# Kernel tuning notes

Hardware: AMD Instinct MI355X
Metric: run time of the kernel (lower is better)

## Reference

```python
import jax, jax.numpy as jnp
import numpy as np

EUCLIDEAN_DIM = 6
B = 1024


def _build_tables(n):
    # CGA: basis vectors e1..en, e+, e-, diagonal metric (+1)*(n+1), (-1)
    d = n + 2
    nb = 1 << d
    metric = [1] * (n + 1) + [-1]
    # clifford orders blades by (grade, lexicographic) == (popcount, bitmask)
    masks = sorted(range(nb), key=lambda m: (bin(m).count('1'), m))
    pos = {m: i for i, m in enumerate(masks)}

    def sign_of(a, b):
        # canonical reordering sign + metric contractions for common vectors
        s = 1
        aa = a >> 1
        cnt = 0
        while aa:
            cnt += bin(aa & b).count('1')
            aa >>= 1
        if cnt & 1:
            s = -s
        common = a & b
        i = 0
        while common:
            if (common & 1) and metric[i] < 0:
                s = -s
            common >>= 1
            i += 1
        return s

    nnz = nb * nb  # every basis-blade product is one signed blade (nondegenerate metric)
    left = np.empty(nnz, np.int32)
    right = np.empty(nnz, np.int32)
    res = np.empty(nnz, np.int32)
    sgn = np.empty(nnz, np.int32)
    t = 0
    for i in range(nb):
        ma = masks[i]
        for j in range(nb):
            mb = masks[j]
            left[t] = i
            right[t] = j
            res[t] = pos[ma ^ mb]
            sgn[t] = sign_of(ma, mb)
            t += 1
    grades = np.array([bin(m).count('1') for m in masks])
    point_mask = np.where(grades == 1)[0].astype(np.int32)           # grade-1 blades
    pseudo = pos[nb - 1]
    motor_mask = np.where((grades % 2 == 0) & (np.arange(nb) != pseudo))[0].astype(np.int32)
    rev = ((-1) ** ((grades * (grades - 1)) // 2)).astype(np.int32)  # reverse signs
    motor_rev = rev[motor_mask]
    return left, right, res, sgn, point_mask, motor_mask, motor_rev


def setup_inputs() -> dict:
    key = jax.random.key(0)
    k1, k2 = jax.random.split(key)
    left, right, res, sgn, pmask, mmask, mrev = _build_tables(EUCLIDEAN_DIM)
    motor = jax.random.normal(k1, (B, mmask.shape[0]), jnp.float32)
    x = jax.random.normal(k2, (B, EUCLIDEAN_DIM), jnp.float32)
    return {
        'motor': motor,
        'x': x,
        'left_idx': jnp.asarray(left),
        'right_idx': jnp.asarray(right),
        'result_idx': jnp.asarray(res),
        'signs': jnp.asarray(sgn),
        'point_mask': jnp.asarray(pmask),
        'motor_mask': jnp.asarray(mmask),
        'motor_reverse_signs': jnp.asarray(mrev),
    }


def _gp(a, b, left_idx, right_idx, result_idx, signs_f, nb):
    # gather-multiply-scatter geometric product (same pattern as torch scatter_add)
    prod = signs_f * a[:, left_idx] * b[:, right_idx]  # (B, nnz)
    return jnp.zeros((a.shape[0], nb), a.dtype).at[:, result_idx].add(prod)


def reference(motor, x, left_idx, right_idx, result_idx, signs, point_mask, motor_mask, motor_reverse_signs):
    n = EUCLIDEAN_DIM
    nb = 1 << (n + 2)
    signs_f = signs.astype(jnp.float32)
    # UPGC encode: X = [x, -0.5 + 0.5|x|^2, 0.5 + 0.5|x|^2]
    h = 0.5 * jnp.sum(x * x, axis=-1, keepdims=True)
    point = jnp.concatenate([x, h - 0.5, h + 0.5], axis=-1)  # (B, n+2)
    Bsz = motor.shape[0]
    motor_full = jnp.zeros((Bsz, nb), jnp.float32).at[:, motor_mask].set(motor)
    point_full = jnp.zeros((Bsz, nb), jnp.float32).at[:, point_mask].set(point)
    motor_rev = motor * motor_reverse_signs.astype(jnp.float32)
    motor_rev_full = jnp.zeros((Bsz, nb), jnp.float32).at[:, motor_mask].set(motor_rev)
    # sandwich product M X M~ via two sparse geometric products
    mx = _gp(motor_full, point_full, left_idx, right_idx, result_idx, signs_f, nb)
    out_full = _gp(mx, motor_rev_full, left_idx, right_idx, result_idx, signs_f, nb)
    transformed = out_full[:, point_mask]  # (B, n+2)
    # UPGC decode: first n components
    return transformed[:, :n]
```

## Files before the change

### kernel.cpp

```cpp
#include <hip/hip_runtime.h>

#define NB      256
#define NMOTOR  127
#define NPOINT  8
#define NDIM    6

__global__ __launch_bounds__(256) void cga_motor_apply(
    const float* __restrict__ motor,
    const float* __restrict__ x,
    const int*   __restrict__ result_idx,
    const int*   __restrict__ signs,
    const int*   __restrict__ point_mask,
    const int*   __restrict__ motor_mask,
    const int*   __restrict__ motor_rev_signs,
    float*       __restrict__ out)
{
    __shared__ float m_full[NB];
    __shared__ float mrev_full[NB];
    __shared__ float mx[NB];
    __shared__ float pval[NPOINT];
    __shared__ int   ppos[NPOINT];
    __shared__ float oacc[NDIM];

    const int b = blockIdx.x;
    const int t = threadIdx.x;

    m_full[t]    = 0.0f;
    mrev_full[t] = 0.0f;
    if (t < NDIM) oacc[t] = 0.0f;
    __syncthreads();

    if (t < NMOTOR) {
        float v  = motor[b * NMOTOR + t];
        int  pos = motor_mask[t];
        m_full[pos]    = v;
        mrev_full[pos] = v * (float)motor_rev_signs[t];
    }
    if (t < NPOINT) ppos[t] = point_mask[t];
    if (t == 0) {
        float h = 0.0f;
        float xv[NDIM];
        #pragma unroll
        for (int k = 0; k < NDIM; ++k) { xv[k] = x[b * NDIM + k]; h += xv[k] * xv[k]; }
        h *= 0.5f;
        #pragma unroll
        for (int k = 0; k < NDIM; ++k) pval[k] = xv[k];
        pval[6] = h - 0.5f;
        pval[7] = h + 0.5f;
    }
    __syncthreads();

    {
        float acc = 0.0f;
        #pragma unroll
        for (int k = 0; k < NPOINT; ++k) {
            int   pp = ppos[k];
            int   m  = result_idx[t * NB + pp];
            float s  = (float)signs[m * NB + pp];
            acc += s * m_full[m] * pval[k];
        }
        mx[t] = acc;
    }
    __syncthreads();

    for (int idx = t; idx < NDIM * NMOTOR; idx += 256) {
        int   r  = idx / NMOTOR;
        int   jm = idx - r * NMOTOR;
        int   rp = ppos[r];
        int   jp = motor_mask[jm];
        int   i  = result_idx[rp * NB + jp];
        float s  = (float)signs[i * NB + jp];
        atomicAdd(&oacc[r], s * mx[i] * mrev_full[jp]);
    }
    __syncthreads();

    if (t < NDIM) out[b * NDIM + t] = oacc[t];
}

extern "C" void kernel_launch(void* const* d_in, const int* in_sizes, int n_in,
                              void* d_out, int out_size, void* d_ws, size_t ws_size,
                              hipStream_t stream) {
    const float* motor      = (const float*)d_in[0];
    const float* x          = (const float*)d_in[1];
    const int*   result_idx = (const int*)d_in[4];
    const int*   signs      = (const int*)d_in[5];
    const int*   point_mask = (const int*)d_in[6];
    const int*   motor_mask = (const int*)d_in[7];
    const int*   mrev       = (const int*)d_in[8];
    float*       out        = (float*)d_out;

    const int Bsz = in_sizes[0] / NMOTOR;
    cga_motor_apply<<<Bsz, 256, 0, stream>>>(motor, x, result_idx, signs,
                                             point_mask, motor_mask, mrev, out);
}
```

Measured before the change: 84.06 us.

## Precompute packed index/sign tables in a prep kernel and reduce with shuffles

Adds a small prep kernel that gathers the needed result indices and signs into a compact packed table in workspace, with the sign stored as the low bit of each index. The main kernel then loads these entries with vector loads instead of doing dependent scattered gathers through the 256x256 result and sign tables. The shared-memory atomicAdd accumulation is replaced by wavefront shuffle reductions, and the point encoding is computed redundantly per thread instead of by a single thread. The cost is an extra kernel launch per call and reliance on the workspace buffer.

```diff
diff --git a/kernel.cpp b/kernel.cpp
--- a/kernel.cpp
+++ b/kernel.cpp
@@ -1,80 +1,131 @@
 #include <hip/hip_runtime.h>
 
-#define NB      256
-#define NMOTOR  127
-#define NPOINT  8
-#define NDIM    6
+#define NB   256
+#define NM   127
+#define NP   8
+#define ND   6
 
-__global__ __launch_bounds__(256) void cga_motor_apply(
+#define FIRST_OFF  0
+#define SECOND_OFF 2048
+#define MP_OFF     3064
+#define PREP_N     3191
+
+__global__ __launch_bounds__(256) void cga_prep(
+    const int* __restrict__ result_idx,
+    const int* __restrict__ signs,
+    const int* __restrict__ point_mask,
+    const int* __restrict__ motor_mask,
+    const int* __restrict__ mrev_signs,
+    int* __restrict__ ws)
+{
+    int e = blockIdx.x * 256 + threadIdx.x;
+    if (e < 2048) {
+        int i  = e >> 3, k = e & 7;
+        int pp = point_mask[k];
+        int m  = result_idx[i * NB + pp];
+        int s  = signs[m * NB + pp];
+        ws[FIRST_OFF + e] = (m << 1) | (s < 0 ? 1 : 0);
+    } else if (e < SECOND_OFF + NM * 8) {
+        int q = e - SECOND_OFF;
+        int j = q >> 3, r = q & 7;
+        int v = 0;
+        if (r < ND) {
+            int rp = point_mask[r];
+            int jp = motor_mask[j];
+            int i  = result_idx[rp * NB + jp];
+            int s  = signs[i * NB + jp];
+            v = (i << 1) | (s < 0 ? 1 : 0);
+        }
+        ws[SECOND_OFF + q] = v;
+    } else if (e < PREP_N) {
+        int j = e - MP_OFF;
+        ws[MP_OFF + j] = (motor_mask[j] << 1) | (mrev_signs[j] < 0 ? 1 : 0);
+    }
+}
+
+__global__ __launch_bounds__(256) void cga_apply(
     const float* __restrict__ motor,
     const float* __restrict__ x,
-    const int*   __restrict__ result_idx,
-    const int*   __restrict__ signs,
-    const int*   __restrict__ point_mask,
-    const int*   __restrict__ motor_mask,
-    const int*   __restrict__ motor_rev_signs,
+    const int*   __restrict__ ws,
     float*       __restrict__ out)
 {
     __shared__ float m_full[NB];
-    __shared__ float mrev_full[NB];
     __shared__ float mx[NB];
-    __shared__ float pval[NPOINT];
-    __shared__ int   ppos[NPOINT];
-    __shared__ float oacc[NDIM];
+    __shared__ float xs[ND];
+    __shared__ float wpart[4][ND];
 
+    const int t = threadIdx.x;
     const int b = blockIdx.x;
-    const int t = threadIdx.x;
 
-    m_full[t]    = 0.0f;
-    mrev_full[t] = 0.0f;
-    if (t < NDIM) oacc[t] = 0.0f;
+    m_full[t] = 0.0f;
+
+    const int4* ft = (const int4*)(ws + FIRST_OFF);
+    int4 f0 = ft[2 * t];
+    int4 f1 = ft[2 * t + 1];
+
+    int   mp = 0;
+    float mv = 0.0f;
+    int4  s0 = {0,0,0,0}, s1 = {0,0,0,0};
+    if (t < NM) {
+        mv = motor[b * NM + t];
+        mp = ws[MP_OFF + t];
+        const int4* st = (const int4*)(ws + SECOND_OFF);
+        s0 = st[2 * t];
+        s1 = st[2 * t + 1];
+    }
+    if (t < ND) xs[t] = x[b * ND + t];
     __syncthreads();
 
-    if (t < NMOTOR) {
-        float v  = motor[b * NMOTOR + t];
-        int  pos = motor_mask[t];
-        m_full[pos]    = v;
-        mrev_full[pos] = v * (float)motor_rev_signs[t];
+    if (t < NM) m_full[mp >> 1] = mv;
+    __syncthreads();
+
+    float pv[NP];
+    float h = 0.0f;
+    #pragma unroll
+    for (int k = 0; k < ND; ++k) { float v = xs[k]; pv[k] = v; h += v * v; }
+    h *= 0.5f;
+    pv[6] = h - 0.5f;
+    pv[7] = h + 0.5f;
+
+    int fe[8] = { f0.x, f0.y, f0.z, f0.w, f1.x, f1.y, f1.z, f1.w };
+    float acc = 0.0f;
+    #pragma unroll
+    for (int k = 0; k < NP; ++k) {
+        int   m = fe[k] >> 1;
+        float v = m_full[m] * pv[k];
+        acc += (fe[k] & 1) ? -v : v;
     }
-    if (t < NPOINT) ppos[t] = point_mask[t];
-    if (t == 0) {
-        float h = 0.0f;
-        float xv[NDIM];
+    mx[t] = acc;
+    __syncthreads();
+
+    float o[ND] = {0,0,0,0,0,0};
+    if (t < NM) {
+        float mr = (mp & 1) ? -mv : mv;
+        int se[ND] = { s0.x, s0.y, s0.z, s0.w, s1.x, s1.y };
         #pragma unroll
-        for (int k = 0; k < NDIM; ++k) { xv[k] = x[b * NDIM + k]; h += xv[k] * xv[k]; }
-        h *= 0.5f;
+        for (int r = 0; r < ND; ++r) {
+            int   i = se[r] >> 1;
+            float v = mx[i] * mr;
+            o[r] += (se[r] & 1) ? -v : v;
+        }
+    }
+
+    #pragma unroll
+    for (int r = 0; r < ND; ++r) {
+        float v = o[r];
         #pragma unroll
-        for (int k = 0; k < NDIM; ++k) pval[k] = xv[k];
-        pval[6] = h - 0.5f;
-        pval[7] = h + 0.5f;
+        for (int d = 32; d >= 1; d >>= 1) v += __shfl_down(v, d, 64);
+        o[r] = v;
+    }
+    const int lane = t & 63, w = t >> 6;
+    if (lane == 0) {
+        #pragma unroll
+        for (int r = 0; r < ND; ++r) wpart[w][r] = o[r];
     }
     __syncthreads();
 
-    {
-        float acc = 0.0f;
-        #pragma unroll
-        for (int k = 0; k < NPOINT; ++k) {
-            int   pp = ppos[k];
-            int   m  = result_idx[t * NB + pp];
-            float s  = (float)signs[m * NB + pp];
-            acc += s * m_full[m] * pval[k];
-        }
-        mx[t] = acc;
-    }
-    __syncthreads();
-
-    for (int idx = t; idx < NDIM * NMOTOR; idx += 256) {
-        int   r  = idx / NMOTOR;
-        int   jm = idx - r * NMOTOR;
-        int   rp = ppos[r];
-        int   jp = motor_mask[jm];
-        int   i  = result_idx[rp * NB + jp];
-        float s  = (float)signs[i * NB + jp];
-        atomicAdd(&oacc[r], s * mx[i] * mrev_full[jp]);
-    }
-    __syncthreads();
-
-    if (t < NDIM) out[b * NDIM + t] = oacc[t];
+    if (t < ND)
+        out[b * ND + t] = wpart[0][t] + wpart[1][t] + wpart[2][t] + wpart[3][t];
 }
 
 extern "C" void kernel_launch(void* const* d_in, const int* in_sizes, int n_in,
@@ -87,9 +138,12 @@
     const int*   point_mask = (const int*)d_in[6];
     const int*   motor_mask = (const int*)d_in[7];
     const int*   mrev       = (const int*)d_in[8];
+    int*         ws         = (int*)d_ws;
     float*       out        = (float*)d_out;
 
-    const int Bsz = in_sizes[0] / NMOTOR;
-    cga_motor_apply<<<Bsz, 256, 0, stream>>>(motor, x, result_idx, signs,
-                                             point_mask, motor_mask, mrev, out);
+    const int Bsz = in_sizes[0] / NM;
+
+    cga_prep<<<(PREP_N + 255) / 256, 256, 0, stream>>>(
+        result_idx, signs, point_mask, motor_mask, mrev, ws);
+    cga_apply<<<Bsz, 256, 0, stream>>>(motor, x, ws, out);
 }
```

Measured after the change: 75.02 us. 1.12x faster.
